# Optimization experiments

Measured on AMD Instinct MI355X. Metric: run time of the kernel, lower is better.

## Reference

```python
import jax, jax.numpy as jnp
import numpy as np

ENC_DIM = 256
DEC_DIM = 256
INT_DIM = 256


def setup_inputs() -> dict:
    key = jax.random.key(0)
    k1, k2, k3, k4, k5 = jax.random.split(key, 5)
    B, T = 64, 2048
    encoder_states = jax.random.normal(k1, (B, T, ENC_DIM), dtype=jnp.float32)
    decoder_state = jax.random.normal(k2, (B, DEC_DIM), dtype=jnp.float32)
    s1 = 1.0 / np.sqrt(ENC_DIM)
    s2 = 1.0 / np.sqrt(DEC_DIM)
    s3 = 1.0 / np.sqrt(INT_DIM)
    w1 = jax.random.uniform(k3, (INT_DIM, ENC_DIM), jnp.float32, -s1, s1)
    w2 = jax.random.uniform(k4, (INT_DIM, DEC_DIM), jnp.float32, -s2, s2)
    v = jax.random.uniform(k5, (1, INT_DIM), jnp.float32, -s3, s3)
    return {"encoder_states": encoder_states, "decoder_state": decoder_state,
            "w1": w1, "w2": w2, "v": v}


def reference(encoder_states, decoder_state, w1, w2, v):
    # scores: v @ tanh(W1 e_t + W2 d) for all t at once
    enc_proj = jnp.einsum('bte,ie->bti', encoder_states, w1)      # [B,T,I]
    dec_proj = jnp.einsum('bd,id->bi', decoder_state, w2)          # [B,I]
    scores = jnp.einsum('bti,oi->bt', jnp.tanh(enc_proj + dec_proj[:, None, :]), v)  # [B,T]
    attention_probs = jax.nn.softmax(scores, axis=1)[:, :, None]   # [B,T,1]
    final_context_vec = jnp.sum(attention_probs * encoder_states, axis=1)  # [B,E]
    return final_context_vec, attention_probs
```

## Files before the change

kernel.cpp:

```cpp
#include <hip/hip_runtime.h>
#include <hip/hip_bf16.h>
#include <math.h>

#define Bq 64
#define Tq 2048
#define Eq 256
#define Dq 256
#define Iq 256

using short8  = __attribute__((ext_vector_type(8))) short;
using floatx4 = __attribute__((ext_vector_type(4))) float;

__device__ __forceinline__ float fast_tanh(float x) {
    float e = __expf(2.0f * x);
    return fmaf(-2.0f, __builtin_amdgcn_rcpf(e + 1.0f), 1.0f);
}

__device__ __forceinline__ ushort f2bf(float x) {
    union { __hip_bfloat16 h; ushort u; } c;
    c.h = __float2bfloat16(x);
    return c.u;
}

__device__ __forceinline__ void async_load16(const void* g, void* l) {
    __builtin_amdgcn_global_load_lds(
        (const __attribute__((address_space(1))) void*)g,
        (__attribute__((address_space(3))) void*)l, 16, 0, 0);
}

__global__ __launch_bounds__(256) void prep_kernel(
    const float* __restrict__ w1, ushort* __restrict__ w1sw,
    const float* __restrict__ dec, const float* __restrict__ w2,
    float* __restrict__ dproj)
{
    if (blockIdx.x < 32) {
        const int kc = blockIdx.x;
        const int i  = threadIdx.x;
        const float* src = w1 + i * Eq + kc * 8;
        float4 f0 = *(const float4*)src;
        float4 f1 = *(const float4*)(src + 4);
        ushort u[8] = { f2bf(f0.x), f2bf(f0.y), f2bf(f0.z), f2bf(f0.w),
                        f2bf(f1.x), f2bf(f1.y), f2bf(f1.z), f2bf(f1.w) };
        *(short8*)&w1sw[(kc * 256 + i) * 8] = *(short8*)u;
    } else {
        const int b = blockIdx.x - 32;
        const int i = threadIdx.x;
        __shared__ float dls[Dq];
        dls[i] = dec[b * Dq + i];
        __syncthreads();
        const float* w2r = w2 + i * Dq;
        float acc = 0.f;
        #pragma unroll 8
        for (int d = 0; d < Dq; d += 4) {
            float4 wv = *(const float4*)&w2r[d];
            float4 dv = *(const float4*)&dls[d];
            acc += wv.x * dv.x + wv.y * dv.y + wv.z * dv.z + wv.w * dv.w;
        }
        dproj[b * Iq + i] = acc;
    }
}

__global__ __launch_bounds__(256, 2) void scores_ctx_kernel(
    const float*  __restrict__ enc,
    const ushort* __restrict__ w1sw,
    const float*  __restrict__ v,
    const float*  __restrict__ dproj,
    float* __restrict__ escore,
    float* __restrict__ ctxp,
    float* __restrict__ denomp)
{
    const int b   = blockIdx.y;
    const int bx  = blockIdx.x;
    const int t0  = bx * 64;
    const int tid = threadIdx.x;
    const int w   = tid >> 6;
    const int l   = tid & 63;
    const int l15 = l & 15;
    const int lq  = l >> 4;

    __shared__ alignas(16) float Af[64 * 256];
    __shared__ float swred[4 * 64];
    __shared__ float redf[4 * 256];

    const float* encB = enc + ((size_t)b * Tq + t0) * Eq;

    #pragma unroll
    for (int q = 0; q < 16; ++q) {
        const int r = w * 16 + q;
        async_load16(encB + (size_t)r * Eq + (l ^ (r & 15)) * 4,
                     &Af[r * 256]);
    }

    float vv[4], dd[4];
    #pragma unroll
    for (int ni = 0; ni < 4; ++ni) {
        const int i = w * 64 + ni * 16 + l15;
        vv[ni] = v[i];
        dd[ni] = dproj[b * Iq + i];
    }

    floatx4 acc[4][4];
    #pragma unroll
    for (int mi = 0; mi < 4; ++mi)
        #pragma unroll
        for (int ni = 0; ni < 4; ++ni)
            acc[mi][ni] = (floatx4)0.f;

    __syncthreads();

    const ushort* vb = w1sw + (w * 64 + l15) * 8 + lq * 2048;

    #pragma unroll
    for (int kk = 0; kk < 8; ++kk) {
        short8 bfv[4];
        #pragma unroll
        for (int ni = 0; ni < 4; ++ni)
            bfv[ni] = *(const short8*)(vb + kk * 4 * 2048 + ni * 128);

        short8 af[4];
        #pragma unroll
        for (int mi = 0; mi < 4; ++mi) {
            const int r  = mi * 16 + l15;
            const int c0 = kk * 8 + lq * 2;
            const int s0 = c0 ^ l15;
            float4 f0 = *(const float4*)&Af[r * 256 + s0 * 4];
            float4 f1 = *(const float4*)&Af[r * 256 + (s0 ^ 1) * 4];
            ushort u[8] = { f2bf(f0.x), f2bf(f0.y), f2bf(f0.z), f2bf(f0.w),
                            f2bf(f1.x), f2bf(f1.y), f2bf(f1.z), f2bf(f1.w) };
            af[mi] = *(short8*)u;
        }

        __builtin_amdgcn_s_setprio(1);
        #pragma unroll
        for (int mi = 0; mi < 4; ++mi)
            #pragma unroll
            for (int ni = 0; ni < 4; ++ni)
                acc[mi][ni] = __builtin_amdgcn_mfma_f32_16x16x32_bf16(
                    af[mi], bfv[ni], acc[mi][ni], 0, 0, 0);
        __builtin_amdgcn_s_setprio(0);
    }

    float part[4][4];
    #pragma unroll
    for (int mi = 0; mi < 4; ++mi)
        #pragma unroll
        for (int r = 0; r < 4; ++r) part[mi][r] = 0.f;

    #pragma unroll
    for (int ni = 0; ni < 4; ++ni) {
        const float vi = vv[ni];
        const float dp = dd[ni];
        #pragma unroll
        for (int mi = 0; mi < 4; ++mi)
            #pragma unroll
            for (int r = 0; r < 4; ++r)
                part[mi][r] += vi * fast_tanh(acc[mi][ni][r] + dp);
    }

    #pragma unroll
    for (int mi = 0; mi < 4; ++mi)
        #pragma unroll
        for (int r = 0; r < 4; ++r) {
            float x = part[mi][r];
            x += __shfl_xor(x, 1); x += __shfl_xor(x, 2);
            x += __shfl_xor(x, 4); x += __shfl_xor(x, 8);
            part[mi][r] = x;
        }
    if (l15 == 0) {
        #pragma unroll
        for (int mi = 0; mi < 4; ++mi)
            #pragma unroll
            for (int r = 0; r < 4; ++r)
                swred[w * 64 + mi * 16 + lq * 4 + r] = part[mi][r];
    }
    __syncthreads();

    float s = swred[l] + swred[64 + l] + swred[128 + l] + swred[192 + l];
    const float es = __expf(s);
    if (w == 0) {
        escore[(size_t)b * Tq + t0 + l] = es;
        float tot = es;
        tot += __shfl_xor(tot, 1);  tot += __shfl_xor(tot, 2);
        tot += __shfl_xor(tot, 4);  tot += __shfl_xor(tot, 8);
        tot += __shfl_xor(tot, 16); tot += __shfl_xor(tot, 32);
        if (l == 0) denomp[bx * Bq + b] = tot;
    }

    const int el = l * 4;
    float4 a = {0.f, 0.f, 0.f, 0.f};
    #pragma unroll 8
    for (int tt = 0; tt < 16; ++tt) {
        const int t  = w * 16 + tt;
        const float pt = __shfl(es, t);
        const int sl = l ^ (t & 15);
        float4 ev = *(const float4*)&Af[t * 256 + sl * 4];
        a.x += pt * ev.x; a.y += pt * ev.y; a.z += pt * ev.z; a.w += pt * ev.w;
    }
    *(float4*)&redf[w * 256 + el] = a;
    __syncthreads();
    if (w == 0) {
        float4 a0 = *(const float4*)&redf[0 * 256 + el];
        float4 a1 = *(const float4*)&redf[1 * 256 + el];
        float4 a2 = *(const float4*)&redf[2 * 256 + el];
        float4 a3 = *(const float4*)&redf[3 * 256 + el];
        float4 o;
        o.x = a0.x + a1.x + a2.x + a3.x;
        o.y = a0.y + a1.y + a2.y + a3.y;
        o.z = a0.z + a1.z + a2.z + a3.z;
        o.w = a0.w + a1.w + a2.w + a3.w;
        *(float4*)&ctxp[((size_t)bx * Bq + b) * Eq + el] = o;
    }
}

__global__ __launch_bounds__(256) void finalize_kernel(
    const float* __restrict__ ctxp, const float* __restrict__ denomp,
    float* __restrict__ probs, float* __restrict__ ctx)
{
    const int b   = blockIdx.x;
    const int tid = threadIdx.x;

    float d = denomp[(tid & 31) * Bq + b];
    d += __shfl_xor(d, 1);  d += __shfl_xor(d, 2);  d += __shfl_xor(d, 4);
    d += __shfl_xor(d, 8);  d += __shfl_xor(d, 16);
    const float inv = 1.0f / d;

    float* prow = probs + (size_t)b * Tq + tid * 8;
    float4 p0 = *(const float4*)(prow + 0);
    float4 p1 = *(const float4*)(prow + 4);
    p0.x *= inv; p0.y *= inv; p0.z *= inv; p0.w *= inv;
    p1.x *= inv; p1.y *= inv; p1.z *= inv; p1.w *= inv;
    *(float4*)(prow + 0) = p0;
    *(float4*)(prow + 4) = p1;

    float s = 0.f;
    #pragma unroll 8
    for (int c = 0; c < 32; ++c)
        s += ctxp[((size_t)c * Bq + b) * Eq + tid];
    ctx[b * Eq + tid] = s * inv;
}

extern "C" void kernel_launch(void* const* d_in, const int* in_sizes, int n_in,
                              void* d_out, int out_size, void* d_ws, size_t ws_size,
                              hipStream_t stream) {
    const float* enc = (const float*)d_in[0];
    const float* dec = (const float*)d_in[1];
    const float* w1  = (const float*)d_in[2];
    const float* w2  = (const float*)d_in[3];
    const float* v   = (const float*)d_in[4];

    float* out   = (float*)d_out;
    float* ctx   = out;
    float* probs = out + Bq * Eq;

    char* ws = (char*)d_ws;
    float*  ctxp   = (float*)ws;
    float*  denomp = (float*)(ws + (32*Bq*Eq)*4);
    float*  dproj  = (float*)(ws + (32*Bq*Eq)*4 + 32*Bq*4);
    ushort* w1sw   = (ushort*)(ws + (32*Bq*Eq)*4 + 32*Bq*4 + Bq*Iq*4);

    prep_kernel<<<dim3(96), dim3(256), 0, stream>>>(w1, w1sw, dec, w2, dproj);
    scores_ctx_kernel<<<dim3(Tq / 64, Bq), dim3(256), 0, stream>>>(
        enc, w1sw, v, dproj, probs, ctxp, denomp);
    finalize_kernel<<<dim3(Bq), dim3(256), 0, stream>>>(ctxp, denomp, probs, ctx);
}
```

Measured before the change: 227.7 us.

## Make scores kernel persistent with double-buffered encoder tiles and register-resident W1

The scores/context kernel now launches 256 blocks of 512 threads. Each block walks 8 consecutive 64-row time tiles for one batch and double-buffers the encoder tile in LDS through async global-to-LDS loads, so the next tile's fetch overlaps the current tile's MFMA and reduction work. Each of the 8 waves holds a 32-column slice of the bf16 W1 fragments in registers for the whole loop instead of reloading them for every tile. In exchange, LDS use doubles to about 128KB per block, register pressure rises, per-tile barriers are added, and there are fewer blocks to hide latency with.

```diff
diff --git a/kernel.cpp b/kernel.cpp
--- a/kernel.cpp
+++ b/kernel.cpp
@@ -60,7 +60,7 @@
     }
 }
 
-__global__ __launch_bounds__(256, 2) void scores_ctx_kernel(
+__global__ __launch_bounds__(512, 2) void scores_ctx_kernel(
     const float*  __restrict__ enc,
     const ushort* __restrict__ w1sw,
     const float*  __restrict__ v,
@@ -69,147 +69,167 @@
     float* __restrict__ ctxp,
     float* __restrict__ denomp)
 {
-    const int b   = blockIdx.y;
-    const int bx  = blockIdx.x;
-    const int t0  = bx * 64;
+    const int p   = blockIdx.x;
+    const int b   = p >> 2;
+    const int bx0 = (p & 3) * 8;
     const int tid = threadIdx.x;
     const int w   = tid >> 6;
     const int l   = tid & 63;
     const int l15 = l & 15;
     const int lq  = l >> 4;
 
-    __shared__ alignas(16) float Af[64 * 256];
-    __shared__ float swred[4 * 64];
-    __shared__ float redf[4 * 256];
-
-    const float* encB = enc + ((size_t)b * Tq + t0) * Eq;
-
+    __shared__ alignas(16) float Af[2][64 * 256];
+    __shared__ float swred[8 * 64];
+    __shared__ float redf[8 * 256];
+
+    const ushort* vb = w1sw + (w * 32 + l15) * 8 + lq * 2048;
+    short8 bP[8][2];
     #pragma unroll
-    for (int q = 0; q < 16; ++q) {
-        const int r = w * 16 + q;
-        async_load16(encB + (size_t)r * Eq + (l ^ (r & 15)) * 4,
-                     &Af[r * 256]);
-    }
-
-    float vv[4], dd[4];
+    for (int kk = 0; kk < 8; ++kk)
+        #pragma unroll
+        for (int ni = 0; ni < 2; ++ni)
+            bP[kk][ni] = *(const short8*)(vb + kk * 8192 + ni * 128);
+
+    float vv[2], dd[2];
     #pragma unroll
-    for (int ni = 0; ni < 4; ++ni) {
-        const int i = w * 64 + ni * 16 + l15;
+    for (int ni = 0; ni < 2; ++ni) {
+        const int i = w * 32 + ni * 16 + l15;
         vv[ni] = v[i];
         dd[ni] = dproj[b * Iq + i];
     }
-
-    floatx4 acc[4][4];
-    #pragma unroll
-    for (int mi = 0; mi < 4; ++mi)
-        #pragma unroll
-        for (int ni = 0; ni < 4; ++ni)
-            acc[mi][ni] = (floatx4)0.f;
-
-    __syncthreads();
-
-    const ushort* vb = w1sw + (w * 64 + l15) * 8 + lq * 2048;
-
-    #pragma unroll
-    for (int kk = 0; kk < 8; ++kk) {
-        short8 bfv[4];
-        #pragma unroll
-        for (int ni = 0; ni < 4; ++ni)
-            bfv[ni] = *(const short8*)(vb + kk * 4 * 2048 + ni * 128);
-
-        short8 af[4];
-        #pragma unroll
-        for (int mi = 0; mi < 4; ++mi) {
-            const int r  = mi * 16 + l15;
-            const int c0 = kk * 8 + lq * 2;
-            const int s0 = c0 ^ l15;
-            float4 f0 = *(const float4*)&Af[r * 256 + s0 * 4];
-            float4 f1 = *(const float4*)&Af[r * 256 + (s0 ^ 1) * 4];
-            ushort u[8] = { f2bf(f0.x), f2bf(f0.y), f2bf(f0.z), f2bf(f0.w),
-                            f2bf(f1.x), f2bf(f1.y), f2bf(f1.z), f2bf(f1.w) };
-            af[mi] = *(short8*)u;
-        }
-
-        __builtin_amdgcn_s_setprio(1);
+    asm volatile("s_waitcnt vmcnt(0)" ::: "memory");
+    __builtin_amdgcn_sched_barrier(0);
+
+    #define STAGE(bxx, buf)                                                  \
+        _Pragma("unroll")                                                    \
+        for (int q = 0; q < 8; ++q) {                                        \
+            const int r = w * 8 + q;                                         \
+            async_load16(enc + ((size_t)b * Tq + (bxx) * 64 + r) * Eq        \
+                             + (l ^ (r & 15)) * 4,                           \
+                         &Af[buf][r * 256]);                                 \
+        }
+
+    STAGE(bx0, 0);
+
+    #pragma unroll 1
+    for (int j = 0; j < 8; ++j) {
+        const int bx  = bx0 + j;
+        const int cur = j & 1;
+
+        if (j < 7) { STAGE(bx + 1, cur ^ 1); }
+        if (j < 7) { asm volatile("s_waitcnt vmcnt(8)" ::: "memory"); }
+        else       { asm volatile("s_waitcnt vmcnt(0)" ::: "memory"); }
+        __builtin_amdgcn_sched_barrier(0);
+        __builtin_amdgcn_s_barrier();
+        __builtin_amdgcn_sched_barrier(0);
+
+        floatx4 acc[4][2];
         #pragma unroll
         for (int mi = 0; mi < 4; ++mi)
             #pragma unroll
-            for (int ni = 0; ni < 4; ++ni)
-                acc[mi][ni] = __builtin_amdgcn_mfma_f32_16x16x32_bf16(
-                    af[mi], bfv[ni], acc[mi][ni], 0, 0, 0);
-        __builtin_amdgcn_s_setprio(0);
+            for (int ni = 0; ni < 2; ++ni)
+                acc[mi][ni] = (floatx4)0.f;
+
+        #pragma unroll
+        for (int kk = 0; kk < 8; ++kk) {
+            short8 af[4];
+            #pragma unroll
+            for (int mi = 0; mi < 4; ++mi) {
+                const int r  = mi * 16 + l15;
+                const int c0 = kk * 8 + lq * 2;
+                const int s0 = c0 ^ l15;
+                float4 f0 = *(const float4*)&Af[cur][r * 256 + s0 * 4];
+                float4 f1 = *(const float4*)&Af[cur][r * 256 + (s0 ^ 1) * 4];
+                ushort u[8] = { f2bf(f0.x), f2bf(f0.y), f2bf(f0.z), f2bf(f0.w),
+                                f2bf(f1.x), f2bf(f1.y), f2bf(f1.z), f2bf(f1.w) };
+                af[mi] = *(short8*)u;
+            }
+            __builtin_amdgcn_s_setprio(1);
+            #pragma unroll
+            for (int mi = 0; mi < 4; ++mi)
+                #pragma unroll
+                for (int ni = 0; ni < 2; ++ni)
+                    acc[mi][ni] = __builtin_amdgcn_mfma_f32_16x16x32_bf16(
+                        af[mi], bP[kk][ni], acc[mi][ni], 0, 0, 0);
+            __builtin_amdgcn_s_setprio(0);
+        }
+
+        float part[4][4];
+        #pragma unroll
+        for (int mi = 0; mi < 4; ++mi)
+            #pragma unroll
+            for (int r = 0; r < 4; ++r) part[mi][r] = 0.f;
+        #pragma unroll
+        for (int ni = 0; ni < 2; ++ni) {
+            const float vi = vv[ni];
+            const float dp = dd[ni];
+            #pragma unroll
+            for (int mi = 0; mi < 4; ++mi)
+                #pragma unroll
+                for (int r = 0; r < 4; ++r)
+                    part[mi][r] += vi * fast_tanh(acc[mi][ni][r] + dp);
+        }
+        #pragma unroll
+        for (int mi = 0; mi < 4; ++mi)
+            #pragma unroll
+            for (int r = 0; r < 4; ++r) {
+                float x = part[mi][r];
+                x += __shfl_xor(x, 1); x += __shfl_xor(x, 2);
+                x += __shfl_xor(x, 4); x += __shfl_xor(x, 8);
+                part[mi][r] = x;
+            }
+        if (l15 == 0) {
+            #pragma unroll
+            for (int mi = 0; mi < 4; ++mi)
+                #pragma unroll
+                for (int r = 0; r < 4; ++r)
+                    swred[w * 64 + mi * 16 + lq * 4 + r] = part[mi][r];
+        }
+        asm volatile("s_waitcnt lgkmcnt(0)" ::: "memory");
+        __builtin_amdgcn_s_barrier();
+        __builtin_amdgcn_sched_barrier(0);
+
+        float s = 0.f;
+        #pragma unroll
+        for (int ww = 0; ww < 8; ++ww) s += swred[ww * 64 + l];
+        const float es = __expf(s);
+        if (w == 0) {
+            escore[(size_t)b * Tq + bx * 64 + l] = es;
+            float tot = es;
+            tot += __shfl_xor(tot, 1);  tot += __shfl_xor(tot, 2);
+            tot += __shfl_xor(tot, 4);  tot += __shfl_xor(tot, 8);
+            tot += __shfl_xor(tot, 16); tot += __shfl_xor(tot, 32);
+            if (l == 0) denomp[bx * Bq + b] = tot;
+        }
+
+        const int el = l * 4;
+        float4 a = {0.f, 0.f, 0.f, 0.f};
+        #pragma unroll
+        for (int tt = 0; tt < 8; ++tt) {
+            const int t  = w * 8 + tt;
+            const float pt = __shfl(es, t);
+            const int sl = l ^ (t & 15);
+            float4 ev = *(const float4*)&Af[cur][t * 256 + sl * 4];
+            a.x += pt * ev.x; a.y += pt * ev.y; a.z += pt * ev.z; a.w += pt * ev.w;
+        }
+        *(float4*)&redf[w * 256 + el] = a;
+        asm volatile("s_waitcnt lgkmcnt(0)" ::: "memory");
+        __builtin_amdgcn_s_barrier();
+        __builtin_amdgcn_sched_barrier(0);
+        if (w == 0) {
+            float4 o = {0.f, 0.f, 0.f, 0.f};
+            #pragma unroll
+            for (int ww = 0; ww < 8; ++ww) {
+                float4 aw = *(const float4*)&redf[ww * 256 + el];
+                o.x += aw.x; o.y += aw.y; o.z += aw.z; o.w += aw.w;
+            }
+            *(float4*)&ctxp[((size_t)bx * Bq + b) * Eq + el] = o;
+        }
+        asm volatile("s_waitcnt lgkmcnt(0)" ::: "memory");
+        __builtin_amdgcn_s_barrier();
+        __builtin_amdgcn_sched_barrier(0);
     }
-
-    float part[4][4];
-    #pragma unroll
-    for (int mi = 0; mi < 4; ++mi)
-        #pragma unroll
-        for (int r = 0; r < 4; ++r) part[mi][r] = 0.f;
-
-    #pragma unroll
-    for (int ni = 0; ni < 4; ++ni) {
-        const float vi = vv[ni];
-        const float dp = dd[ni];
-        #pragma unroll
-        for (int mi = 0; mi < 4; ++mi)
-            #pragma unroll
-            for (int r = 0; r < 4; ++r)
-                part[mi][r] += vi * fast_tanh(acc[mi][ni][r] + dp);
-    }
-
-    #pragma unroll
-    for (int mi = 0; mi < 4; ++mi)
-        #pragma unroll
-        for (int r = 0; r < 4; ++r) {
-            float x = part[mi][r];
-            x += __shfl_xor(x, 1); x += __shfl_xor(x, 2);
-            x += __shfl_xor(x, 4); x += __shfl_xor(x, 8);
-            part[mi][r] = x;
-        }
-    if (l15 == 0) {
-        #pragma unroll
-        for (int mi = 0; mi < 4; ++mi)
-            #pragma unroll
-            for (int r = 0; r < 4; ++r)
-                swred[w * 64 + mi * 16 + lq * 4 + r] = part[mi][r];
-    }
-    __syncthreads();
-
-    float s = swred[l] + swred[64 + l] + swred[128 + l] + swred[192 + l];
-    const float es = __expf(s);
-    if (w == 0) {
-        escore[(size_t)b * Tq + t0 + l] = es;
-        float tot = es;
-        tot += __shfl_xor(tot, 1);  tot += __shfl_xor(tot, 2);
-        tot += __shfl_xor(tot, 4);  tot += __shfl_xor(tot, 8);
-        tot += __shfl_xor(tot, 16); tot += __shfl_xor(tot, 32);
-        if (l == 0) denomp[bx * Bq + b] = tot;
-    }
-
-    const int el = l * 4;
-    float4 a = {0.f, 0.f, 0.f, 0.f};
-    #pragma unroll 8
-    for (int tt = 0; tt < 16; ++tt) {
-        const int t  = w * 16 + tt;
-        const float pt = __shfl(es, t);
-        const int sl = l ^ (t & 15);
-        float4 ev = *(const float4*)&Af[t * 256 + sl * 4];
-        a.x += pt * ev.x; a.y += pt * ev.y; a.z += pt * ev.z; a.w += pt * ev.w;
-    }
-    *(float4*)&redf[w * 256 + el] = a;
-    __syncthreads();
-    if (w == 0) {
-        float4 a0 = *(const float4*)&redf[0 * 256 + el];
-        float4 a1 = *(const float4*)&redf[1 * 256 + el];
-        float4 a2 = *(const float4*)&redf[2 * 256 + el];
-        float4 a3 = *(const float4*)&redf[3 * 256 + el];
-        float4 o;
-        o.x = a0.x + a1.x + a2.x + a3.x;
-        o.y = a0.y + a1.y + a2.y + a3.y;
-        o.z = a0.z + a1.z + a2.z + a3.z;
-        o.w = a0.w + a1.w + a2.w + a3.w;
-        *(float4*)&ctxp[((size_t)bx * Bq + b) * Eq + el] = o;
-    }
+    #undef STAGE
 }
 
 __global__ __launch_bounds__(256) void finalize_kernel(
@@ -254,12 +274,12 @@
 
     char* ws = (char*)d_ws;
     float*  ctxp   = (float*)ws;
-    float*  denomp = (float*)(ws + (32*Bq*Eq)*4);
-    float*  dproj  = (float*)(ws + (32*Bq*Eq)*4 + 32*Bq*4);
-    ushort* w1sw   = (ushort*)(ws + (32*Bq*Eq)*4 + 32*Bq*4 + Bq*Iq*4);
+    float*  denomp = (float*)(ws + 2097152);
+    float*  dproj  = (float*)(ws + 2097152 + 8192);
+    ushort* w1sw   = (ushort*)(ws + 2097152 + 8192 + 65536);
 
     prep_kernel<<<dim3(96), dim3(256), 0, stream>>>(w1, w1sw, dec, w2, dproj);
-    scores_ctx_kernel<<<dim3(Tq / 64, Bq), dim3(256), 0, stream>>>(
+    scores_ctx_kernel<<<dim3(256), dim3(512), 0, stream>>>(
         enc, w1sw, v, dproj, probs, ctxp, denomp);
     finalize_kernel<<<dim3(Bq), dim3(256), 0, stream>>>(ctxp, denomp, probs, ctx);
 }
```

Result: no change. 231.9 us (+1.8%).
